# Optimization experiments

Measured on AMD Instinct MI355X. Metric: run time of the kernel, lower is better.

Reference implementation:

```python
import jax, jax.numpy as jnp
from jax import lax
import numpy as np

B, T, F_IN = 256, 128, 16
H, L, OUT = 512, 3, 16  # hidden_size, rnn_depth, dim_state*2


def setup_inputs() -> dict:
    key = jax.random.key(0)
    ks = jax.random.split(key, 5)
    scale_in = 1.0 / np.sqrt(F_IN)
    scale_h = 1.0 / np.sqrt(2 * H)
    return {
        "x": jax.random.normal(ks[0], (B, T, F_IN), jnp.float32),
        "proj_w": jax.random.normal(ks[1], (F_IN, H), jnp.float32) * scale_in,
        "proj_b": jnp.zeros((H,), jnp.float32),
        "lstm_w": jax.random.normal(ks[2], (L, 2 * H, 4 * H), jnp.float32) * scale_h,
        "lstm_b": jnp.zeros((L, 4 * H), jnp.float32),
        "out_w": jax.random.normal(ks[3], (H, OUT), jnp.float32) * (1.0 / np.sqrt(H)),
        "out_b": jnp.zeros((OUT,), jnp.float32),
    }


def reference(x, proj_w, proj_b, lstm_w, lstm_b, out_w, out_b):
    # x: [B, T, F_in]
    b, t, _ = x.shape
    n_layers, _, h4 = lstm_w.shape
    h = h4 // 4

    # Projection + relu -> all LSTM layers see H-dim inputs
    xp = jax.nn.relu(jnp.einsum("btf,fh->bth", x, proj_w) + proj_b)  # [B,T,H]

    def step(carry, xt):
        hs_prev, cs_prev = carry  # each [L, B, H]
        inp = xt  # [B, H]
        hs, cs = [], []
        for l in range(n_layers):
            gated = jnp.concatenate([inp, hs_prev[l]], axis=-1) @ lstm_w[l] + lstm_b[l]
            i, g, f, o = jnp.split(gated, 4, axis=-1)
            c_new = jax.nn.sigmoid(f + 1.0) * cs_prev[l] + jax.nn.sigmoid(i) * jnp.tanh(g)
            h_new = jax.nn.sigmoid(o) * jnp.tanh(c_new)
            hs.append(h_new)
            cs.append(c_new)
            # relu between layers (rnn_activation), not after the last layer
            inp = jax.nn.relu(h_new) if l < n_layers - 1 else h_new
        return (jnp.stack(hs), jnp.stack(cs)), inp

    zeros = jnp.zeros((n_layers, b, h), xp.dtype)
    xs = jnp.swapaxes(xp, 0, 1)  # [T, B, H] for scan over time
    _, ys = lax.scan(step, (zeros, zeros), xs)
    y = jnp.swapaxes(ys, 0, 1)  # [B, T, H]
    return jnp.einsum("bth,ho->bto", y, out_w) + out_b
```

## Files before the change

### kernel.cpp

```cpp
#include <hip/hip_runtime.h>


typedef __attribute__((ext_vector_type(8)))  short bf16x8;
typedef __attribute__((ext_vector_type(16))) float f32x16;
typedef __attribute__((ext_vector_type(8)))  unsigned short us8;

#define B_  256
#define T_  128
#define FIN 16
#define H_  512
#define G4  2048
#define SLAB 131072
#define MF(A,B,C) __builtin_amdgcn_mfma_f32_32x32x16_bf16(A,B,C,0,0,0)

static __device__ __forceinline__ float bf2f(unsigned short u){
  return __uint_as_float(((unsigned)u) << 16);
}
static __device__ __forceinline__ unsigned short f2bf(float f){
  unsigned u = __float_as_uint(f);
  u += 0x7fffu + ((u >> 16) & 1u);
  return (unsigned short)(u >> 16);
}
static __device__ __forceinline__ float sigm(float x){ return 1.f/(1.f + __expf(-x)); }
static __device__ __forceinline__ float tanh_(float x){ return 1.f - 2.f/(__expf(2.f*x) + 1.f); }

static __device__ __forceinline__ void wave_wait(const int* slotbase, int v){
  int guard = 0;
  for (;;){
    int s = __hip_atomic_load((const int*)(slotbase + (threadIdx.x & 31)),
                              __ATOMIC_RELAXED, __HIP_MEMORY_SCOPE_AGENT);
    if (__all(s >= v) || guard++ > (1 << 17)) break;
    __builtin_amdgcn_s_sleep(2);
  }
  asm volatile("" ::: "memory");
}


__global__ __launch_bounds__(256) void k_wconv(const float* __restrict__ w,
                                               unsigned short* __restrict__ wfo){
  long idx = (long)blockIdx.x*256 + threadIdx.x;
  int lane = (int)(idx & 63);
  int s    = (int)((idx >> 6) & 63);
  int Jb   = (int)((idx >> 12) & 63);
  int l    = (int)(idx >> 18);
  int jp = Jb*32 + (lane & 31);
  int co = (jp & 3)*512 + (jp >> 2);
  int k0 = s*16 + (lane >> 5)*8;
  us8 o;
  #pragma unroll
  for (int e = 0; e < 8; ++e)
    o[e] = f2bf(w[((long)(l*1024 + k0 + e))*2048 + co]);
  *(us8*)(wfo + idx*8) = o;
}

__global__ __launch_bounds__(256) void k_xp(const float* __restrict__ x,
                                            const float* __restrict__ pw,
                                            const float* __restrict__ pb,
                                            unsigned short* __restrict__ xpt){
  __shared__ float sw[FIN*H_];
  __shared__ float sb[H_];
  int tid = threadIdx.x;
  for (int i = tid; i < FIN*H_; i += 256) sw[i] = pw[i];
  for (int i = tid; i < H_;     i += 256) sb[i] = pb[i];
  __syncthreads();
  int r0 = blockIdx.x * 64;
  int c0 = tid * 2;
  int s  = c0 >> 4, kl = c0 & 15;
  for (int rr = 0; rr < 64; ++rr){
    int r = r0 + rr;
    int b = r >> 7, t = r & 127;
    const float* xr = x + (long)r*FIN;
    float a0 = sb[c0], a1 = sb[c0+1];
    #pragma unroll
    for (int f = 0; f < FIN; ++f){
      float xv = xr[f];
      a0 += xv * sw[f*H_ + c0];
      a1 += xv * sw[f*H_ + c0 + 1];
    }
    ushort2 tmp;
    tmp.x = f2bf(fmaxf(a0, 0.f));
    tmp.y = f2bf(fmaxf(a1, 0.f));
    long off = (long)t*SLAB
             + ((((b>>7)*4 + ((b>>5)&3))*32 + s) << 9)
             + ((b&31) + ((kl>>3)<<5))*8 + (kl&7);
    *(ushort2*)(xpt + off) = tmp;
  }
}

__global__ __launch_bounds__(256) void k_out(const unsigned short* __restrict__ ring,
                                             const float* __restrict__ ow,
                                             const float* __restrict__ ob,
                                             float* __restrict__ dout){
  __shared__ float sw[H_*16];
  int tid = threadIdx.x;
  for (int i = tid; i < H_*16; i += 256) sw[i] = ow[i];
  __syncthreads();
  int r0 = blockIdx.x * 16;
  int rr = tid >> 4, o = tid & 15;
  int r = r0 + rr;
  int b = r >> 7, t = r & 127;
  long tb = ((long)t*3 + 2)*SLAB + (((b>>7)*4 + ((b>>5)&3)) << 14);
  float acc = ob[o];
  for (int k8 = 0; k8 < 64; ++k8){
    long off = tb + ((long)(k8 >> 1) << 9) + ((b&31) + ((k8&1)<<5))*8;
    us8 v = *(const us8*)(ring + off);
    #pragma unroll
    for (int e = 0; e < 8; ++e) acc += bf2f(v[e]) * sw[(k8*8 + e)*16 + o];
  }
  dout[(long)r*16 + o] = acc;
}


#define DMA1(I) { \
  __builtin_amdgcn_global_load_lds( \
    (const __attribute__((address_space(1))) void*)(gsrc + (I)*512), \
    (__attribute__((address_space(3))) void*)(actb + (((I) % 24) << 10)), 16, 0, 0); }

#define ISSUE4(G) { DMA1((G)*4+0) DMA1((G)*4+1) DMA1((G)*4+2) DMA1((G)*4+3) }

#define WVM(N) { asm volatile("s_waitcnt vmcnt(" #N ")" ::: "memory"); \
                 __builtin_amdgcn_sched_barrier(0); }
#define LGK0   { asm volatile("s_waitcnt lgkmcnt(0)" ::: "memory"); \
                 __builtin_amdgcn_sched_barrier(0); }

#define CONS(I, RELU) { \
  bf16x8 w0 = *(const bf16x8*)(Wl + (((I)*64 + lane) << 4)); \
  bf16x8 w1 = *(const bf16x8*)(Wl + (32768 + (((I)*64 + lane) << 4))); \
  bf16x8 b  = *(const bf16x8*)(actb + (((I) % 24) << 10) + (lane << 4)); \
  if (RELU){ _Pragma("unroll") for (int e = 0; e < 8; ++e) if (b[e] < 0) b[e] = 0; } \
  a0 = MF(w0, b, a0); a1 = MF(w1, b, a1); }

#define CONSR(I) { \
  bf16x8 b = *(const bf16x8*)(actb + (((I) % 24) << 10) + (lane << 4)); \
  a0 = MF(wr0[I], b, a0); a1 = MF(wr1[I], b, a1); }

#define CONS4(G, R)  { CONS((G)*4+0,R) CONS((G)*4+1,R) CONS((G)*4+2,R) CONS((G)*4+3,R) }
#define CONSR4(G)    { CONSR((G)*4+0) CONSR((G)*4+1) CONSR((G)*4+2) CONSR((G)*4+3) }

#define GEMM5_L(R) { \
  ISSUE4(0) ISSUE4(1) ISSUE4(2) ISSUE4(3) ISSUE4(4) \
  WVM(16) CONS4(0,R) LGK0 ISSUE4(5) \
  WVM(16) CONS4(1,R) LGK0 ISSUE4(6) \
  WVM(16) CONS4(2,R) LGK0 ISSUE4(7) \
  WVM(16) CONS4(3,R) \
  WVM(12) CONS4(4,R) \
  WVM(8)  CONS4(5,R) \
  WVM(4)  CONS4(6,R) \
  WVM(0)  CONS4(7,R) \
  LGK0 }

#define GEMM5_R { \
  ISSUE4(0) ISSUE4(1) ISSUE4(2) ISSUE4(3) ISSUE4(4) \
  WVM(16) CONSR4(0) LGK0 ISSUE4(5) \
  WVM(16) CONSR4(1) LGK0 ISSUE4(6) \
  WVM(16) CONSR4(2) LGK0 ISSUE4(7) \
  WVM(16) CONSR4(3) \
  WVM(12) CONSR4(4) \
  WVM(8)  CONSR4(5) \
  WVM(4)  CONSR4(6) \
  WVM(0)  CONSR4(7) \
  LGK0 }

#define CELL1(A, JB) { _Pragma("unroll") \
  for (int q = 0; q < 4; ++q){ \
    float iv = A[4*q+0], gv = A[4*q+1], fv = A[4*q+2], ov = A[4*q+3]; \
    float cp = cs##JB[q]; \
    float cn = sigm(fv + 1.f)*cp + sigm(iv)*tanh_(gv); \
    float hn = sigm(ov)*tanh_(cn); \
    cs##JB[q] = cn; \
    hst[l31*24 + JB*8 + 2*q + l5] = f2bf(hn); } }

__global__ __launch_bounds__(256, 1) void k_rnn(
    const unsigned short* __restrict__ wf, const float* __restrict__ lb,
    unsigned short* ownring, unsigned short* crossring,
    const unsigned short* __restrict__ xpt,
    int* stepslots, int* xcdslots, int sepAvail)
{
  extern __shared__ unsigned char Wl[];
  const int bid = blockIdx.x;
  const int g = bid & 7;
  if (g >= 6) return;
  const int l = g >> 1, mg = g & 1;
  const int n = bid >> 3;
  const int tid = threadIdx.x;
  const int lane = tid & 63;
  const int wv = tid >> 6;
  const int l5 = lane >> 5, l31 = lane & 31;
  const int tilebase = (mg*4 + wv) << 5;
  unsigned char* actb = Wl + 65536 + wv*24576;
  unsigned short* hst = (unsigned short*)actb;

  const unsigned short* wbase = wf + ((long)(l*64 + n*2))*4096*8;

  {
    us8* dst = (us8*)Wl;
    const us8* sj0 = (const us8*)wbase;
    const us8* sj1 = (const us8*)(wbase + 32768);
    for (int i = tid; i < 4096; i += 256)
      dst[i] = (i < 2048) ? sj0[i] : sj1[i - 2048];
  }
  bf16x8 wr0[32], wr1[32];
  #pragma unroll
  for (int i = 0; i < 32; ++i){
    wr0[i] = *(const bf16x8*)(wbase + ((long)((32+i)*64 + lane))*8);
    wr1[i] = *(const bf16x8*)(wbase + 32768 + ((long)((32+i)*64 + lane))*8);
  }
  f32x16 bias0, bias1;
  #pragma unroll
  for (int r = 0; r < 16; ++r){
    int hc0 = (n*2 + 0)*8 + 2*(r>>2) + l5;
    int hc1 = (n*2 + 1)*8 + 2*(r>>2) + l5;
    bias0[r] = lb[l*G4 + (r&3)*512 + hc0];
    bias1[r] = lb[l*G4 + (r&3)*512 + hc1];
  }
  float cs0[4] = {0.f,0.f,0.f,0.f}, cs1[4] = {0.f,0.f,0.f,0.f};
  __syncthreads();

  unsigned myxcd = 0;
  asm volatile("s_getreg_b32 %0, hwreg(HW_REG_XCC_ID)" : "=s"(myxcd));
  if (tid == 0)
    __hip_atomic_store(xcdslots + g*32 + n, 1 + (int)myxcd,
                       __ATOMIC_RELAXED, __HIP_MEMORY_SCOPE_AGENT);
  int uni;
  {
    int guard = 0, s = 0;
    for (;;){
      s = __hip_atomic_load((const int*)(xcdslots + g*32 + (lane & 31)),
                            __ATOMIC_RELAXED, __HIP_MEMORY_SCOPE_AGENT);
      if (__all(s >= 1) || guard++ > (1 << 17)) break;
      __builtin_amdgcn_s_sleep(2);
    }
    uni = __all(s == 1 + (int)myxcd);
    asm volatile("" ::: "memory");
  }
  const int ownSep = (sepAvail && uni) ? 1 : 0;
  const unsigned short* ownr = ownSep ? ownring : crossring;

  const int* sOwn  = stepslots + g*32;
  const int* sPrev = stepslots + (g - 2)*32;
  int* myFlag = stepslots + g*32 + n;

  for (int t = 0; t < T_; ++t){
    f32x16 a0 = bias0, a1 = bias1;

    if (l == 0){
      const unsigned short* gsrc = xpt + (long)t*SLAB + ((long)tilebase << 9)
                                 + lane*8;
      GEMM5_L(0)
    } else {
      wave_wait(sPrev, t + 1);
      const unsigned short* gsrc = crossring + ((long)t*3 + (l-1))*SLAB
                                 + ((long)tilebase << 9) + lane*8;
      GEMM5_L(1)
    }
    if (t > 0){
      wave_wait(sOwn, t);
      const unsigned short* gsrc = ownr + ((long)(t-1)*3 + l)*SLAB
                                 + ((long)tilebase << 9) + lane*8;
      GEMM5_R
    }

    CELL1(a0, 0)
    CELL1(a1, 1)
    asm volatile("s_waitcnt lgkmcnt(0)" ::: "memory");
    __builtin_amdgcn_sched_barrier(0);
    {
      us8 v = *(const us8*)(hst + l31*24 + l5*8);
      long off = ((long)t*3 + l)*SLAB + ((long)(tilebase + n) << 9) + lane*8;
      if (ownSep) *(us8*)(ownring + off) = v;
      *(volatile us8*)(crossring + off) = v;
    }
    __syncthreads();
    if (tid == 0)
      __hip_atomic_store(myFlag, t + 1, __ATOMIC_RELAXED, __HIP_MEMORY_SCOPE_AGENT);
  }
}


__global__ __launch_bounds__(256) void k_wconv0(const float* __restrict__ w,
                                                unsigned short* __restrict__ wf){
  long d8 = ((long)blockIdx.x*256 + threadIdx.x) * 8;
  int lane = (int)((d8 >> 3) & 63);
  int s    = (int)((d8 >> 9) & 31);
  int J    = (int)((d8 >> 14) & 127);
  int l    = (int)(d8 >> 21);
  int jj = lane & 15, khi = lane >> 4;
  int jp = J*16 + jj;
  int co = (jp & 3)*512 + (jp >> 2);
  int kbase = s*32 + khi*8;
  us8 o;
  #pragma unroll
  for (int e = 0; e < 8; ++e)
    o[e] = f2bf(w[((long)(l*1024 + kbase + e))*2048 + co]);
  *(us8*)(wf + d8) = o;
}

__global__ void k_iout(float* __restrict__ dout, const float* __restrict__ ob){
  int i = blockIdx.x*256 + threadIdx.x;
  if (i < B_*T_*16) dout[i] = ob[i & 15];
}

__global__ __launch_bounds__(256, 2) void k_stage0(
    const float* __restrict__ x, const float* __restrict__ pw, const float* __restrict__ pb,
    const unsigned short* __restrict__ wf, const float* __restrict__ lb,
    const float* __restrict__ ow, float* __restrict__ dout,
    float* __restrict__ cbuf, unsigned short* __restrict__ hb,
    int t, int l)
{
  __shared__ unsigned char Ab[32*2048];
  __shared__ float gsm[32*36];
  __shared__ float xrow[32*16];
  __shared__ float hcell[32*8];

  const int tid = threadIdx.x;
  const int bid = blockIdx.x;
  const int m = bid >> 6;
  const int n = ((bid & 7) << 3) | ((bid >> 3) & 7);
  const int pwr = t & 1, prd = pwr ^ 1;
  const int bg0 = m * 32;

  {
    const unsigned short* src = hb + (((long)prd*3 + l)*256 + bg0)*512;
    for (int i = 0; i < 8; ++i){
      int cid = tid + 256*i;
      int row = cid >> 6, cc = cid & 63;
      us8 v = *(const us8*)(src + (long)row*512 + cc*8);
      *(us8*)(Ab + ((row*2048 + 1024 + cc*16) ^ ((row & 7) << 4))) = v;
    }
  }
  if (l > 0){
    const unsigned short* src = hb + (((long)pwr*3 + (l-1))*256 + bg0)*512;
    for (int i = 0; i < 8; ++i){
      int cid = tid + 256*i;
      int row = cid >> 6, cc = cid & 63;
      us8 v = *(const us8*)(src + (long)row*512 + cc*8);
      #pragma unroll
      for (int e = 0; e < 8; ++e) v[e] = (v[e] & 0x8000u) ? (unsigned short)0 : v[e];
      *(us8*)(Ab + ((row*2048 + cc*16) ^ ((row & 7) << 4))) = v;
    }
  } else {
    {
      int e2 = tid*2;
      int br = e2 >> 4, f = e2 & 15;
      const float* xr = x + ((long)(bg0 + br)*T_ + t)*FIN;
      xrow[e2] = xr[f]; xrow[e2+1] = xr[f+1];
    }
    __syncthreads();
    for (int i = 0; i < 8; ++i){
      int cid = tid + 256*i;
      int row = cid >> 6, cc = cid & 63;
      int c0 = cc*8;
      us8 vv;
      #pragma unroll
      for (int j = 0; j < 8; ++j){
        float a = pb[c0 + j];
        #pragma unroll
        for (int f = 0; f < FIN; ++f) a += xrow[row*16 + f] * pw[f*H_ + c0 + j];
        vv[j] = f2bf(fmaxf(a, 0.f));
      }
      *(us8*)(Ab + ((row*2048 + cc*16) ^ ((row & 7) << 4))) = vv;
    }
  }
  __syncthreads();

  const int lane = tid & 63, wid = tid >> 6;
  const int wm = wid >> 1, wn = wid & 1;
  const int J = n*2 + wn;
  const int arow = wm*16 + (lane & 15);
  const unsigned abase = (unsigned)arow*2048 + ((lane >> 4) << 4);
  const unsigned axor = (unsigned)((arow & 7) << 4);
  const unsigned short* bp = wf + ((((long)l*128 + J)*32)*64 + lane)*8;

  typedef __attribute__((ext_vector_type(4))) float f32x4;
  f32x4 acc = {0.f, 0.f, 0.f, 0.f};
  #pragma unroll
  for (int s = 0; s < 32; ++s){
    bf16x8 af = *(const bf16x8*)(Ab + ((abase + s*64) ^ axor));
    bf16x8 bfr = *(const bf16x8*)(bp + (long)s*512);
    acc = __builtin_amdgcn_mfma_f32_16x16x32_bf16(af, bfr, acc, 0, 0, 0);
  }
  {
    int colb = wn*16 + (lane & 15);
    int rowb = wm*16 + ((lane >> 4) << 2);
    #pragma unroll
    for (int r = 0; r < 4; ++r) gsm[(rowb + r)*36 + colb] = acc[r];
  }
  __syncthreads();

  {
    int bl = tid >> 3, hc = tid & 7;
    float4 g4 = *(float4*)(&gsm[bl*36 + hc*4]);
    int hcol = n*8 + hc;
    int bgl = bg0 + bl;
    float iv = g4.x + lb[l*G4 + hcol];
    float gv = g4.y + lb[l*G4 + 512 + hcol];
    float fv = g4.z + lb[l*G4 + 1024 + hcol];
    float ov = g4.w + lb[l*G4 + 1536 + hcol];
    long coff = ((long)l*256 + bgl)*512 + hcol;
    float cp = cbuf[coff];
    float cn = sigm(fv + 1.f)*cp + sigm(iv)*tanh_(gv);
    float hn = sigm(ov)*tanh_(cn);
    cbuf[coff] = cn;
    hb[(((long)pwr*3 + l)*256 + bgl)*512 + hcol] = f2bf(hn);
    if (l == 2) hcell[bl*8 + hc] = hn;
  }
  if (l == 2){
    __syncthreads();
    #pragma unroll
    for (int q = 0; q < 2; ++q){
      int oid = tid + 256*q;
      int bl = oid >> 4, o = oid & 15;
      float a = 0.f;
      #pragma unroll
      for (int hc = 0; hc < 8; ++hc) a += hcell[bl*8 + hc] * ow[(n*8 + hc)*16 + o];
      atomicAdd(dout + ((long)(bg0 + bl)*T_ + t)*16 + o, a);
    }
  }
}


extern "C" void kernel_launch(void* const* d_in, const int* in_sizes, int n_in,
                              void* d_out, int out_size, void* d_ws, size_t ws_size,
                              hipStream_t stream)
{
  const float* x  = (const float*)d_in[0];
  const float* pw = (const float*)d_in[1];
  const float* pb = (const float*)d_in[2];
  const float* lw = (const float*)d_in[3];
  const float* lb = (const float*)d_in[4];
  const float* ow = (const float*)d_in[5];
  const float* ob = (const float*)d_in[6];
  float* dout = (float*)d_out;

  const size_t RING = 128ull*3*SLAB*2;
  char* ws = (char*)d_ws;
  size_t off = 0;
  auto carve = [&](size_t bytes){ char* p = ws + off; off += (bytes + 255) & ~(size_t)255; return p; };

  unsigned short* wf    = (unsigned short*)carve(3ull*64*4096*8*2);
  unsigned short* cross = (unsigned short*)carve(RING);
  unsigned short* xpt   = (unsigned short*)carve(128ull*SLAB*2);
  int*            steps = (int*)carve(1024);
  int*            xcds  = (int*)carve(1024);
  size_t need_mid = off;
  unsigned short* own   = (unsigned short*)carve(RING);
  size_t need_lux = off;

  int mode = (ws_size >= need_lux) ? 2 : (ws_size >= need_mid ? 1 : 0);
  if (mode){
    if (hipFuncSetAttribute((const void*)k_rnn,
                            hipFuncAttributeMaxDynamicSharedMemorySize,
                            163840) != hipSuccess)
      mode = 0;
  }

  if (mode){
    int sepAvail = (mode == 2) ? 1 : 0;
    unsigned short* ownp = sepAvail ? own : cross;
    hipMemsetAsync(steps, 0, 2048, stream);
    k_wconv<<<3072, 256, 0, stream>>>(lw, wf);
    k_xp<<<512, 256, 0, stream>>>(x, pw, pb, xpt);
    k_rnn<<<256, 256, 163840, stream>>>(wf, lb, ownp, cross, xpt,
                                        steps, xcds, sepAvail);
    k_out<<<2048, 256, 0, stream>>>(cross, ow, ob, dout);
  } else {
    size_t o2 = 0;
    auto carve2 = [&](size_t bytes){ char* p = ws + o2; o2 += (bytes + 255) & ~(size_t)255; return p; };
    unsigned short* wf0   = (unsigned short*)carve2(3ull*1024*2048*2);
    float*          cbuf0 = (float*)carve2(3ull*256*512*4);
    unsigned short* hbuf0 = (unsigned short*)carve2(2ull*3*256*512*2);
    hipMemsetAsync(cbuf0, 0, 3ull*256*512*4 + 2ull*3*256*512*2, stream);
    k_wconv0<<<3072, 256, 0, stream>>>(lw, wf0);
    k_iout<<<2048, 256, 0, stream>>>(dout, ob);
    for (int t = 0; t < T_; ++t)
      for (int l = 0; l < 3; ++l)
        k_stage0<<<512, 256, 0, stream>>>(x, pw, pb, wf0, lb, ow, dout,
                                          cbuf0, hbuf0, t, l);
  }
}
```

Measured before the change: 1.181 ms.

## Load activations directly into registers instead of async global-to-LDS DMA

Replaces the global_load_lds ring-buffer staging of activation tiles, with its explicit vmcnt/lgkmcnt waits, by plain global loads into two banks of eight register vectors that are double-buffered against the MFMA chains. This removes the LDS round trip and the LDS read per MFMA, and shrinks the per-wave LDS scratch to the hidden-state staging area. In exchange it uses many more VGPRs, and the load/compute overlap now depends on compiler scheduling instead of hand-placed waits.

```diff
diff --git a/kernel.cpp b/kernel.cpp
--- a/kernel.cpp
+++ b/kernel.cpp
@@ -111,55 +111,36 @@
 }
 
 
-#define DMA1(I) { \
-  __builtin_amdgcn_global_load_lds( \
-    (const __attribute__((address_space(1))) void*)(gsrc + (I)*512), \
-    (__attribute__((address_space(3))) void*)(actb + (((I) % 24) << 10)), 16, 0, 0); }
-
-#define ISSUE4(G) { DMA1((G)*4+0) DMA1((G)*4+1) DMA1((G)*4+2) DMA1((G)*4+3) }
-
-#define WVM(N) { asm volatile("s_waitcnt vmcnt(" #N ")" ::: "memory"); \
-                 __builtin_amdgcn_sched_barrier(0); }
-#define LGK0   { asm volatile("s_waitcnt lgkmcnt(0)" ::: "memory"); \
-                 __builtin_amdgcn_sched_barrier(0); }
-
-#define CONS(I, RELU) { \
+#define LDB8(V, G) { \
+  V##0 = *(const bf16x8*)(gsrc + ((G)*8+0)*512); \
+  V##1 = *(const bf16x8*)(gsrc + ((G)*8+1)*512); \
+  V##2 = *(const bf16x8*)(gsrc + ((G)*8+2)*512); \
+  V##3 = *(const bf16x8*)(gsrc + ((G)*8+3)*512); \
+  V##4 = *(const bf16x8*)(gsrc + ((G)*8+4)*512); \
+  V##5 = *(const bf16x8*)(gsrc + ((G)*8+5)*512); \
+  V##6 = *(const bf16x8*)(gsrc + ((G)*8+6)*512); \
+  V##7 = *(const bf16x8*)(gsrc + ((G)*8+7)*512); }
+
+#define KL(V, I, RELU) { \
   bf16x8 w0 = *(const bf16x8*)(Wl + (((I)*64 + lane) << 4)); \
   bf16x8 w1 = *(const bf16x8*)(Wl + (32768 + (((I)*64 + lane) << 4))); \
-  bf16x8 b  = *(const bf16x8*)(actb + (((I) % 24) << 10) + (lane << 4)); \
+  bf16x8 b = V; \
   if (RELU){ _Pragma("unroll") for (int e = 0; e < 8; ++e) if (b[e] < 0) b[e] = 0; } \
   a0 = MF(w0, b, a0); a1 = MF(w1, b, a1); }
 
-#define CONSR(I) { \
-  bf16x8 b = *(const bf16x8*)(actb + (((I) % 24) << 10) + (lane << 4)); \
-  a0 = MF(wr0[I], b, a0); a1 = MF(wr1[I], b, a1); }
-
-#define CONS4(G, R)  { CONS((G)*4+0,R) CONS((G)*4+1,R) CONS((G)*4+2,R) CONS((G)*4+3,R) }
-#define CONSR4(G)    { CONSR((G)*4+0) CONSR((G)*4+1) CONSR((G)*4+2) CONSR((G)*4+3) }
-
-#define GEMM5_L(R) { \
-  ISSUE4(0) ISSUE4(1) ISSUE4(2) ISSUE4(3) ISSUE4(4) \
-  WVM(16) CONS4(0,R) LGK0 ISSUE4(5) \
-  WVM(16) CONS4(1,R) LGK0 ISSUE4(6) \
-  WVM(16) CONS4(2,R) LGK0 ISSUE4(7) \
-  WVM(16) CONS4(3,R) \
-  WVM(12) CONS4(4,R) \
-  WVM(8)  CONS4(5,R) \
-  WVM(4)  CONS4(6,R) \
-  WVM(0)  CONS4(7,R) \
-  LGK0 }
-
-#define GEMM5_R { \
-  ISSUE4(0) ISSUE4(1) ISSUE4(2) ISSUE4(3) ISSUE4(4) \
-  WVM(16) CONSR4(0) LGK0 ISSUE4(5) \
-  WVM(16) CONSR4(1) LGK0 ISSUE4(6) \
-  WVM(16) CONSR4(2) LGK0 ISSUE4(7) \
-  WVM(16) CONSR4(3) \
-  WVM(12) CONSR4(4) \
-  WVM(8)  CONSR4(5) \
-  WVM(4)  CONSR4(6) \
-  WVM(0)  CONSR4(7) \
-  LGK0 }
+#define KR(V, I) { a0 = MF(wr0[I], V, a0); a1 = MF(wr1[I], V, a1); }
+
+#define KL8(V, G, R) { KL(V##0,(G)*8+0,R) KL(V##1,(G)*8+1,R) KL(V##2,(G)*8+2,R) \
+  KL(V##3,(G)*8+3,R) KL(V##4,(G)*8+4,R) KL(V##5,(G)*8+5,R) \
+  KL(V##6,(G)*8+6,R) KL(V##7,(G)*8+7,R) }
+#define KR8(V, G) { KR(V##0,(G)*8+0) KR(V##1,(G)*8+1) KR(V##2,(G)*8+2) \
+  KR(V##3,(G)*8+3) KR(V##4,(G)*8+4) KR(V##5,(G)*8+5) \
+  KR(V##6,(G)*8+6) KR(V##7,(G)*8+7) }
+
+#define GEMML(R) { LDB8(bA,0) LDB8(bB,1) KL8(bA,0,R) LDB8(bA,2) \
+                   KL8(bB,1,R) LDB8(bB,3) KL8(bA,2,R) KL8(bB,3,R) }
+#define GEMMR    { LDB8(bA,0) LDB8(bB,1) KR8(bA,0) LDB8(bA,2) \
+                   KR8(bB,1) LDB8(bB,3) KR8(bA,2) KR8(bB,3) }
 
 #define CELL1(A, JB) { _Pragma("unroll") \
   for (int q = 0; q < 4; ++q){ \
@@ -187,8 +168,7 @@
   const int wv = tid >> 6;
   const int l5 = lane >> 5, l31 = lane & 31;
   const int tilebase = (mg*4 + wv) << 5;
-  unsigned char* actb = Wl + 65536 + wv*24576;
-  unsigned short* hst = (unsigned short*)actb;
+  unsigned short* hst = (unsigned short*)(Wl + 65536 + wv*4096);
 
   const unsigned short* wbase = wf + ((long)(l*64 + n*2))*4096*8;
 
@@ -240,24 +220,27 @@
   const int* sPrev = stepslots + (g - 2)*32;
   int* myFlag = stepslots + g*32 + n;
 
+  bf16x8 bA0,bA1,bA2,bA3,bA4,bA5,bA6,bA7;
+  bf16x8 bB0,bB1,bB2,bB3,bB4,bB5,bB6,bB7;
+
   for (int t = 0; t < T_; ++t){
     f32x16 a0 = bias0, a1 = bias1;
 
     if (l == 0){
       const unsigned short* gsrc = xpt + (long)t*SLAB + ((long)tilebase << 9)
                                  + lane*8;
-      GEMM5_L(0)
+      GEMML(0)
     } else {
       wave_wait(sPrev, t + 1);
       const unsigned short* gsrc = crossring + ((long)t*3 + (l-1))*SLAB
                                  + ((long)tilebase << 9) + lane*8;
-      GEMM5_L(1)
+      GEMML(1)
     }
     if (t > 0){
       wave_wait(sOwn, t);
       const unsigned short* gsrc = ownr + ((long)(t-1)*3 + l)*SLAB
                                  + ((long)tilebase << 9) + lane*8;
-      GEMM5_R
+      GEMMR
     }
 
     CELL1(a0, 0)
```

New measurement: 2.195 ms. 1.86x slower.
